# Optimization experiments

Hardware: AMD Instinct MI355X
Metric: run time of the kernel (lower is better)

The kernel has to match this reference:

```python
import jax, jax.numpy as jnp
import numpy as np

GAMMA_EPS = 0.05
ALPHA_POS = 4.0
ALPHA_NEG = 1.0

N, D, K_CLUSTERS = 262144, 128, 256


def setup_inputs() -> dict:
    key = jax.random.key(0)
    k1, k2, k3 = jax.random.split(key, 3)
    Xemb = jax.random.normal(k1, (N, D), dtype=jnp.float32)
    scores = jax.random.normal(k2, (N, K_CLUSTERS), dtype=jnp.float32)
    labels = jax.random.randint(k3, (N,), 0, K_CLUSTERS, dtype=jnp.int64)
    h_bias = jnp.asarray(0.1, dtype=jnp.float32)  # nn.Parameter(init_bias)
    return {"Xemb": Xemb, "scores": scores, "labels": labels,
            "h_bias": h_bias, "K": K_CLUSTERS}


def _bcl_forward(Xemb, scores, h_bias, labels, K):
    # labels are uniform in [0, K), so sorted unique labels == arange(K)
    # and the loop's k-index equals the label itself (pos_idx = labels).
    bias = jax.nn.softplus(h_bias)
    pos_bias = bias
    neg_bias = 9.0 * bias + GAMMA_EPS

    # scatter-mean centroids per cluster, then L2-normalize each centroid
    sums = jax.ops.segment_sum(Xemb, labels, num_segments=K)          # [K, D]
    counts = jax.ops.segment_sum(jnp.ones((Xemb.shape[0],), Xemb.dtype),
                                 labels, num_segments=K)              # [K]
    centroids = sums / counts[:, None]
    centroids = centroids / jnp.linalg.norm(centroids, axis=1, keepdims=True)

    x2 = jnp.sum(Xemb * Xemb, axis=1, keepdims=True)                  # [N, 1]
    c2 = jnp.sum(centroids * centroids, axis=1)                       # [K]
    XC_dist = x2 + c2[None, :] - 2.0 * (Xemb @ centroids.T)           # [N, K]

    # positive distance: gather own-cluster column
    pos_distances = jnp.take_along_axis(XC_dist, labels[:, None], axis=1)[:, 0]
    pos_sample_loss = jax.nn.relu(pos_distances - pos_bias)

    # min over negative clusters (exclude own column)
    own = jax.nn.one_hot(labels, K, dtype=jnp.bool_)
    min_neg = jnp.min(jnp.where(own, jnp.inf, XC_dist), axis=1)
    neg_sample_loss = jax.nn.relu(neg_bias - min_neg)

    pos_loss = jnp.mean(pos_sample_loss) * ALPHA_POS
    neg_loss = jnp.mean(neg_sample_loss) * ALPHA_NEG
    return jnp.stack([pos_loss, neg_loss])  # [ctrd_pos, ctrd_neg]


def reference(Xemb, scores, labels, h_bias, K):
    return _bcl_forward(Xemb, scores, h_bias, labels, K)
```

## Files before the change

kernel.cpp:

```cpp
#include <hip/hip_runtime.h>
#include <hip/hip_bf16.h>

#define DD 128
#define KK 256
#define TS 256
#define ROWB 136
#define SPB1 1024

typedef __attribute__((ext_vector_type(8))) short short8;
typedef __attribute__((ext_vector_type(4))) float f32x4;

static __device__ __forceinline__ unsigned short f2bf(float f) {
    unsigned int u = __float_as_uint(f);
    return (unsigned short)((u + 0x7fffu + ((u >> 16) & 1u)) >> 16);
}
static __device__ __forceinline__ float bf2f(unsigned short h) {
    return __uint_as_float(((unsigned int)h) << 16);
}

template<int MODE>
__global__ __launch_bounds__(1024) void k_stage1_gather(
    const float* __restrict__ X, const int* __restrict__ labels,
    float* __restrict__ partial)
{
    __shared__ int lab[SPB1];
    __shared__ int idx[SPB1];
    __shared__ int hist[KK];
    __shared__ int start[KK + 1];
    __shared__ int cursor[KK];

    const int tid  = threadIdx.x;
    const int lane = tid & 63;
    const int wave = tid >> 6;
    const int base = blockIdx.x * SPB1;

    if (tid < KK) hist[tid] = 0;
    __syncthreads();
    {
        const int l = labels[base + tid];
        lab[tid] = l;
        atomicAdd(&hist[l], 1);
    }
    __syncthreads();
    if (wave == 0) {
        const int h0 = hist[4*lane], h1 = hist[4*lane+1];
        const int h2 = hist[4*lane+2], h3 = hist[4*lane+3];
        const int s = h0 + h1 + h2 + h3;
        int t = s;
#pragma unroll
        for (int d = 1; d < 64; d <<= 1) { const int u = __shfl_up(t, d); if (lane >= d) t += u; }
        const int e = t - s;
        start[4*lane]   = e;
        start[4*lane+1] = e + h0;
        start[4*lane+2] = e + h0 + h1;
        start[4*lane+3] = e + h0 + h1 + h2;
        if (lane == 63) start[KK] = t;
    }
    __syncthreads();
    if (tid < KK) cursor[tid] = start[tid];
    __syncthreads();
    {
        const int pos = atomicAdd(&cursor[lab[tid]], 1);
        idx[pos] = tid;
    }
    __syncthreads();

    for (int c = wave; c < KK; c += 16) {
        const int s0 = start[c], s1 = start[c + 1];
        float2 acc = make_float2(0.f, 0.f);
        if (s1 > s0) {
            int n0 = idx[s0];
            float2 v = *(const float2*)(X + (size_t)(base + n0) * DD + 2 * lane);
            for (int i = s0 + 1; i < s1; ++i) {
                const int n1 = idx[i];
                const float2 v1 = *(const float2*)(X + (size_t)(base + n1) * DD + 2 * lane);
                acc.x += v.x; acc.y += v.y;
                n0 = n1; v = v1;
            }
            acc.x += v.x; acc.y += v.y;
        }
        if (MODE == 2) {
            atomicAdd(&partial[(size_t)c * DD + 2 * lane],     acc.x);
            atomicAdd(&partial[(size_t)c * DD + 2 * lane + 1], acc.y);
        } else {
            *(float2*)(partial + ((size_t)blockIdx.x * KK + c) * DD + 2 * lane) = acc;
        }
    }
}

__global__ void k_stage2(const float* __restrict__ partial, int nparts,
                         unsigned short* __restrict__ centb)
{
    const int k = blockIdx.x;
    const int t = threadIdx.x;
    const int d = t & (DD - 1);
    const int slice = t >> 7;
    float s = 0.f;
    for (int b = slice; b < nparts; b += 4)
        s += partial[((size_t)b * KK + k) * DD + d];
    __shared__ float red[4][DD];
    red[slice][d] = s;
    __syncthreads();
    float v = 0.f;
    if (t < DD) v = red[0][d] + red[1][d] + red[2][d] + red[3][d];
    float sq = v * v;
#pragma unroll
    for (int m = 32; m > 0; m >>= 1) sq += __shfl_xor(sq, m);
    __shared__ float wsum[8];
    if ((t & 63) == 0) wsum[t >> 6] = sq;
    __syncthreads();
    if (t < DD) centb[k * DD + d] = f2bf(v * rsqrtf(wsum[0] + wsum[1]));
}

__global__ __launch_bounds__(1024, 4) void k_stage3(
    const float* __restrict__ Xf, const int* __restrict__ labels,
    const unsigned short* __restrict__ centb,
    const float* __restrict__ hbias, float* __restrict__ loss, int spb)
{
    __shared__ unsigned short Cl[KK * ROWB];
    __shared__ unsigned short Xl[TS * ROWB];
    __shared__ int   labs[TS];
    __shared__ float lred[32];

    const int tid = threadIdx.x;
    const float hb = *hbias;
    const float bias = (hb > 20.f) ? hb : log1pf(__expf(hb));
    const float pos_bias = bias;
    const float neg_bias = 9.f * bias + 0.05f;

    const uint4* csrc = (const uint4*)centb;
    for (int c = tid; c < KK * DD / 8; c += 1024) {
        const int row = c >> 4;
        const int col = (c & 15) << 3;
        *(uint4*)(&Cl[row * ROWB + col]) = csrc[c];
    }

    const int lane = tid & 63;
    const int wave = tid >> 6;
    const int m15  = lane & 15;
    const int q    = lane >> 4;
    const int kq   = q << 3;
    const int base = blockIdx.x * spb;
    float pos_acc = 0.f, neg_acc = 0.f;

    for (int t0 = 0; t0 < spb; t0 += TS) {
        __syncthreads();
        const float4* xsrc = (const float4*)(Xf + (size_t)(base + t0) * DD);
        for (int c = tid; c < TS * DD / 4; c += 1024) {
            const int row = c >> 5;
            const int col = (c & 31) << 2;
            const float4 v = xsrc[c];
            ushort4 pk = make_ushort4(f2bf(v.x), f2bf(v.y), f2bf(v.z), f2bf(v.w));
            *(ushort4*)(&Xl[row * ROWB + col]) = pk;
        }
        if (tid < TS) labs[tid] = labels[base + t0 + tid];
        __syncthreads();

        short8 afrag[4];
        const int arow = (wave << 4) + m15;
#pragma unroll
        for (int s = 0; s < 4; ++s)
            afrag[s] = *(const short8*)(&Xl[arow * ROWB + (s << 5) + kq]);

        float x2p = 0.f;
#pragma unroll
        for (int s = 0; s < 4; ++s)
#pragma unroll
            for (int j = 0; j < 8; ++j) {
                const float e = bf2f((unsigned short)afrag[s][j]);
                x2p = fmaf(e, e, x2p);
            }
        x2p += __shfl_xor(x2p, 16);
        x2p += __shfl_xor(x2p, 32);

        f32x4 acc[16];
#pragma unroll
        for (int t = 0; t < 16; ++t) acc[t] = (f32x4){0.f, 0.f, 0.f, 0.f};
#pragma unroll
        for (int t = 0; t < 16; ++t) {
            const int brow = (t << 4) + m15;
#pragma unroll
            for (int s = 0; s < 4; ++s) {
                const short8 bfrag = *(const short8*)(&Cl[brow * ROWB + (s << 5) + kq]);
                acc[t] = __builtin_amdgcn_mfma_f32_16x16x32_bf16(afrag[s], bfrag, acc[t], 0, 0, 0);
            }
        }

#pragma unroll
        for (int r = 0; r < 4; ++r) {
            const int ml = (wave << 4) + (q << 2) + r;
            const int l  = labs[ml];
            const float x2 = __shfl(x2p, (q << 2) + r, 16);
            float posd = -1e30f, negd = -1e30f;
#pragma unroll
            for (int t = 0; t < 16; ++t) {
                const int cl = (t << 4) + m15;
                const float v = acc[t][r];
                const bool isp = (cl == l);
                posd = isp ? v : posd;
                negd = isp ? negd : fmaxf(negd, v);
            }
#pragma unroll
            for (int m = 1; m < 16; m <<= 1) {
                posd = fmaxf(posd, __shfl_xor(posd, m));
                negd = fmaxf(negd, __shfl_xor(negd, m));
            }
            if (m15 == 0) {
                const float pd = x2 + 1.0f - 2.f * posd;
                const float nd = x2 + 1.0f - 2.f * negd;
                pos_acc += fmaxf(pd - pos_bias, 0.f);
                neg_acc += fmaxf(neg_bias - nd, 0.f);
            }
        }
    }

#pragma unroll
    for (int m = 32; m > 0; m >>= 1) {
        pos_acc += __shfl_xor(pos_acc, m);
        neg_acc += __shfl_xor(neg_acc, m);
    }
    if (lane == 0) { lred[wave] = pos_acc; lred[16 + wave] = neg_acc; }
    __syncthreads();
    if (tid == 0) {
        float p = 0.f, n = 0.f;
#pragma unroll
        for (int w = 0; w < 16; ++w) { p += lred[w]; n += lred[16 + w]; }
        atomicAdd(&loss[0], p);
        atomicAdd(&loss[1], n);
    }
}

__global__ void k_final(const float* __restrict__ loss, float* __restrict__ out, float invN)
{
    if (threadIdx.x == 0) {
        out[0] = 4.0f * loss[0] * invN;
        out[1] = loss[1] * invN;
    }
}

extern "C" void kernel_launch(void* const* d_in, const int* in_sizes, int n_in,
                              void* d_out, int out_size, void* d_ws, size_t ws_size,
                              hipStream_t stream)
{
    const float* X      = (const float*)d_in[0];
    const int*   labels = (const int*)d_in[2];
    const float* hbias  = (const float*)d_in[3];
    float* out = (float*)d_out;
    const int N = in_sizes[0] / DD;
    const int G = N / SPB1;

    char* ws = (char*)d_ws;
    const size_t offC    = 256;
    const size_t offPart = offC + (size_t)KK * DD * 2;
    const size_t szPart  = (size_t)G * KK * DD * 4;

    float*          loss    = (float*)ws;
    unsigned short* centb   = (unsigned short*)(ws + offC);
    float*          partial = (float*)(ws + offPart);

    const int mode   = (ws_size >= offPart + szPart) ? 0 : 2;
    const int nparts = (mode == 2) ? 1 : G;

    hipMemsetAsync(loss, 0, 2 * sizeof(float), stream);
    if (mode == 2) hipMemsetAsync(partial, 0, (size_t)KK * DD * 4, stream);

    if (mode == 0) k_stage1_gather<0><<<G, 1024, 0, stream>>>(X, labels, partial);
    else           k_stage1_gather<2><<<G, 1024, 0, stream>>>(X, labels, partial);

    k_stage2<<<KK, 512, 0, stream>>>(partial, nparts, centb);

    k_stage3<<<G, 1024, 0, stream>>>(X, labels, centb, hbias, loss, N / G);

    k_final<<<1, 64, 0, stream>>>(loss, out, 1.0f / (float)N);
}
```

Measured before the change: 479.9 us.

## Emit bf16 X and row norms in stage1; stage3 uses 32x32 MFMA with prefetch

Stage 1 now writes a bf16 copy of X and per-row squared norms while it gathers rows for the centroid sums. Stage 3 reads that half-size bf16 copy and prefetches the next tile into registers, so it no longer converts fp32 X itself. It also moves from 16x16x32 to 32x32x16 MFMA with 512-thread blocks and uses DPP/swizzle max reductions. The extra writes in stage 1 and the larger workspace are paid to cut stage-3 traffic and conversion work; the x2 norm now comes from fp32 values rather than bf16-rounded ones.

```diff
diff --git a/kernel.cpp b/kernel.cpp
--- a/kernel.cpp
+++ b/kernel.cpp
@@ -8,20 +8,33 @@
 #define SPB1 1024
 
 typedef __attribute__((ext_vector_type(8))) short short8;
-typedef __attribute__((ext_vector_type(4))) float f32x4;
+typedef __attribute__((ext_vector_type(16))) float f32x16;
 
 static __device__ __forceinline__ unsigned short f2bf(float f) {
     unsigned int u = __float_as_uint(f);
     return (unsigned short)((u + 0x7fffu + ((u >> 16) & 1u)) >> 16);
 }
-static __device__ __forceinline__ float bf2f(unsigned short h) {
-    return __uint_as_float(((unsigned int)h) << 16);
+
+template<int CTRL>
+static __device__ __forceinline__ float mdpp_max(float x) {
+    const int xi = __builtin_bit_cast(int, x);
+    const int yi = __builtin_amdgcn_update_dpp(xi, xi, CTRL, 0xF, 0xF, false);
+    return fmaxf(x, __builtin_bit_cast(float, yi));
+}
+static __device__ __forceinline__ float redmax32(float x) {
+    x = mdpp_max<0xB1>(x);
+    x = mdpp_max<0x4E>(x);
+    x = mdpp_max<0x124>(x);
+    x = mdpp_max<0x128>(x);
+    const int yi = __builtin_amdgcn_ds_swizzle(__builtin_bit_cast(int, x), 0x401F);
+    return fmaxf(x, __builtin_bit_cast(float, yi));
 }
 
 template<int MODE>
 __global__ __launch_bounds__(1024) void k_stage1_gather(
     const float* __restrict__ X, const int* __restrict__ labels,
-    float* __restrict__ partial)
+    float* __restrict__ partial, unsigned int* __restrict__ Xbf,
+    float* __restrict__ x2g)
 {
     __shared__ int lab[SPB1];
     __shared__ int idx[SPB1];
@@ -75,9 +88,25 @@
                 const int n1 = idx[i];
                 const float2 v1 = *(const float2*)(X + (size_t)(base + n1) * DD + 2 * lane);
                 acc.x += v.x; acc.y += v.y;
+                if (MODE == 0) {
+                    Xbf[(size_t)(base + n0) * (DD/2) + lane] =
+                        ((unsigned)f2bf(v.y) << 16) | (unsigned)f2bf(v.x);
+                    float p = v.x*v.x + v.y*v.y;
+#pragma unroll
+                    for (int m = 32; m > 0; m >>= 1) p += __shfl_xor(p, m);
+                    if (lane == 0) x2g[base + n0] = p;
+                }
                 n0 = n1; v = v1;
             }
             acc.x += v.x; acc.y += v.y;
+            if (MODE == 0) {
+                Xbf[(size_t)(base + n0) * (DD/2) + lane] =
+                    ((unsigned)f2bf(v.y) << 16) | (unsigned)f2bf(v.x);
+                float p = v.x*v.x + v.y*v.y;
+#pragma unroll
+                for (int m = 32; m > 0; m >>= 1) p += __shfl_xor(p, m);
+                if (lane == 0) x2g[base + n0] = p;
+            }
         }
         if (MODE == 2) {
             atomicAdd(&partial[(size_t)c * DD + 2 * lane],     acc.x);
@@ -112,102 +141,148 @@
     if (t < DD) centb[k * DD + d] = f2bf(v * rsqrtf(wsum[0] + wsum[1]));
 }
 
-__global__ __launch_bounds__(1024, 4) void k_stage3(
-    const float* __restrict__ Xf, const int* __restrict__ labels,
+template<int XB>
+__global__ __launch_bounds__(512, 2) void k_stage3(
+    const float* __restrict__ Xf, const unsigned int* __restrict__ Xbf,
+    const int* __restrict__ labels, const float* __restrict__ x2g,
     const unsigned short* __restrict__ centb,
     const float* __restrict__ hbias, float* __restrict__ loss, int spb)
 {
-    __shared__ unsigned short Cl[KK * ROWB];
-    __shared__ unsigned short Xl[TS * ROWB];
-    __shared__ int   labs[TS];
-    __shared__ float lred[32];
-
-    const int tid = threadIdx.x;
+    __shared__ __align__(16) unsigned short Cl[KK * ROWB];
+    __shared__ __align__(16) unsigned short Xl[TS * ROWB];
+    __shared__ __align__(16) int   labsS[TS];
+    __shared__ __align__(16) float x2S[TS];
+    __shared__ float lred[16];
+
+    const int tid  = threadIdx.x;
+    const int lane = tid & 63;
+    const int wave = tid >> 6;
+    const int l31  = lane & 31;
+    const int half = lane >> 5;
+    const int base = blockIdx.x * spb;
+
     const float hb = *hbias;
     const float bias = (hb > 20.f) ? hb : log1pf(__expf(hb));
     const float pos_bias = bias;
     const float neg_bias = 9.f * bias + 0.05f;
 
-    const uint4* csrc = (const uint4*)centb;
-    for (int c = tid; c < KK * DD / 8; c += 1024) {
-        const int row = c >> 4;
-        const int col = (c & 15) << 3;
-        *(uint4*)(&Cl[row * ROWB + col]) = csrc[c];
-    }
-
-    const int lane = tid & 63;
-    const int wave = tid >> 6;
-    const int m15  = lane & 15;
-    const int q    = lane >> 4;
-    const int kq   = q << 3;
-    const int base = blockIdx.x * spb;
+    {
+        const uint4* csrc = (const uint4*)centb;
+        for (int c = tid; c < KK * DD / 8; c += 512) {
+            const int row = c >> 4, col = (c & 15) << 3;
+            *(uint4*)(&Cl[row * ROWB + col]) = csrc[c];
+        }
+    }
+
+    uint4 buf[8];
+    int labr = 0; float x2r = 0.f;
+    if (XB) {
+        const uint4* xs = (const uint4*)Xbf;
+        const size_t gb = (size_t)base << 4;
+#pragma unroll
+        for (int i = 0; i < 8; ++i) buf[i] = xs[gb + tid + (i << 9)];
+        if (tid < TS) { labr = labels[base + tid]; x2r = x2g[base + tid]; }
+    }
+
     float pos_acc = 0.f, neg_acc = 0.f;
 
     for (int t0 = 0; t0 < spb; t0 += TS) {
         __syncthreads();
-        const float4* xsrc = (const float4*)(Xf + (size_t)(base + t0) * DD);
-        for (int c = tid; c < TS * DD / 4; c += 1024) {
-            const int row = c >> 5;
-            const int col = (c & 31) << 2;
-            const float4 v = xsrc[c];
-            ushort4 pk = make_ushort4(f2bf(v.x), f2bf(v.y), f2bf(v.z), f2bf(v.w));
-            *(ushort4*)(&Xl[row * ROWB + col]) = pk;
-        }
-        if (tid < TS) labs[tid] = labels[base + t0 + tid];
-        __syncthreads();
-
-        short8 afrag[4];
-        const int arow = (wave << 4) + m15;
-#pragma unroll
-        for (int s = 0; s < 4; ++s)
-            afrag[s] = *(const short8*)(&Xl[arow * ROWB + (s << 5) + kq]);
-
-        float x2p = 0.f;
-#pragma unroll
-        for (int s = 0; s < 4; ++s)
-#pragma unroll
-            for (int j = 0; j < 8; ++j) {
-                const float e = bf2f((unsigned short)afrag[s][j]);
-                x2p = fmaf(e, e, x2p);
-            }
-        x2p += __shfl_xor(x2p, 16);
-        x2p += __shfl_xor(x2p, 32);
-
-        f32x4 acc[16];
-#pragma unroll
-        for (int t = 0; t < 16; ++t) acc[t] = (f32x4){0.f, 0.f, 0.f, 0.f};
-#pragma unroll
-        for (int t = 0; t < 16; ++t) {
-            const int brow = (t << 4) + m15;
-#pragma unroll
-            for (int s = 0; s < 4; ++s) {
-                const short8 bfrag = *(const short8*)(&Cl[brow * ROWB + (s << 5) + kq]);
-                acc[t] = __builtin_amdgcn_mfma_f32_16x16x32_bf16(afrag[s], bfrag, acc[t], 0, 0, 0);
-            }
-        }
-
-#pragma unroll
-        for (int r = 0; r < 4; ++r) {
-            const int ml = (wave << 4) + (q << 2) + r;
-            const int l  = labs[ml];
-            const float x2 = __shfl(x2p, (q << 2) + r, 16);
-            float posd = -1e30f, negd = -1e30f;
-#pragma unroll
-            for (int t = 0; t < 16; ++t) {
-                const int cl = (t << 4) + m15;
-                const float v = acc[t][r];
-                const bool isp = (cl == l);
-                posd = isp ? v : posd;
-                negd = isp ? negd : fmaxf(negd, v);
-            }
-#pragma unroll
-            for (int m = 1; m < 16; m <<= 1) {
-                posd = fmaxf(posd, __shfl_xor(posd, m));
-                negd = fmaxf(negd, __shfl_xor(negd, m));
-            }
-            if (m15 == 0) {
-                const float pd = x2 + 1.0f - 2.f * posd;
-                const float nd = x2 + 1.0f - 2.f * negd;
+
+        if (XB) {
+#pragma unroll
+            for (int i = 0; i < 8; ++i) {
+                const int c = tid + (i << 9);
+                const int row = c >> 4, col = (c & 15) << 3;
+                *(uint4*)(&Xl[row * ROWB + col]) = buf[i];
+            }
+            if (tid < TS) { labsS[tid] = labr; x2S[tid] = x2r; }
+            if (t0 + TS < spb) {
+                const uint4* xs = (const uint4*)Xbf;
+                const size_t gb = (size_t)(base + t0 + TS) << 4;
+#pragma unroll
+                for (int i = 0; i < 8; ++i) buf[i] = xs[gb + tid + (i << 9)];
+                if (tid < TS) {
+                    labr = labels[base + t0 + TS + tid];
+                    x2r  = x2g[base + t0 + TS + tid];
+                }
+            }
+            __syncthreads();
+        } else {
+            const float4* xsrc = (const float4*)(Xf + (size_t)(base + t0) * DD);
+            for (int c = tid; c < TS * DD / 4; c += 512) {
+                const int row = c >> 5, col = (c & 31) << 2;
+                const float4 v = xsrc[c];
+                ushort4 pk = make_ushort4(f2bf(v.x), f2bf(v.y), f2bf(v.z), f2bf(v.w));
+                *(ushort4*)(&Xl[row * ROWB + col]) = pk;
+            }
+            if (tid < TS) labsS[tid] = labels[base + t0 + tid];
+            __syncthreads();
+            {
+                const int s  = tid >> 1, h = tid & 1;
+                float p = 0.f;
+#pragma unroll
+                for (int c = 0; c < 8; ++c) {
+                    const short8 w = *(const short8*)(&Xl[s * ROWB + (h << 6) + (c << 3)]);
+#pragma unroll
+                    for (int j = 0; j < 8; ++j) {
+                        const float e = __uint_as_float(((unsigned)(unsigned short)w[j]) << 16);
+                        p = fmaf(e, e, p);
+                    }
+                }
+                p += __shfl_xor(p, 1);
+                if (h == 0 && s < TS) x2S[s] = p;
+            }
+            __syncthreads();
+        }
+
+        short8 af[8];
+        const int arow = (wave << 5) + l31;
+#pragma unroll
+        for (int s = 0; s < 8; ++s)
+            af[s] = *(const short8*)(&Xl[arow * ROWB + (s << 4) + (half << 3)]);
+
+        int la[16]; float xv[16];
+#pragma unroll
+        for (int g = 0; g < 4; ++g) {
+            const int r0 = (wave << 5) + (g << 3) + (half << 2);
+            const int4   L  = *(const int4*)(&labsS[r0]);
+            const float4 Xq = *(const float4*)(&x2S[r0]);
+            la[4*g+0] = L.x;  la[4*g+1] = L.y;  la[4*g+2] = L.z;  la[4*g+3] = L.w;
+            xv[4*g+0] = Xq.x; xv[4*g+1] = Xq.y; xv[4*g+2] = Xq.z; xv[4*g+3] = Xq.w;
+        }
+
+        float posc[16], negc[16];
+#pragma unroll
+        for (int r = 0; r < 16; ++r) { posc[r] = -1e30f; negc[r] = -1e30f; }
+
+#pragma unroll
+        for (int t = 0; t < 8; ++t) {
+            f32x16 acc;
+#pragma unroll
+            for (int r = 0; r < 16; ++r) acc[r] = 0.f;
+#pragma unroll
+            for (int s = 0; s < 8; ++s) {
+                const short8 bf = *(const short8*)(&Cl[(t*32 + l31) * ROWB + (s << 4) + (half << 3)]);
+                acc = __builtin_amdgcn_mfma_f32_32x32x16_bf16(af[s], bf, acc, 0, 0, 0);
+            }
+            const int myc = (t << 5) + l31;
+#pragma unroll
+            for (int r = 0; r < 16; ++r) {
+                const float v = acc[r];
+                const bool own = (la[r] == myc);
+                negc[r] = own ? negc[r] : fmaxf(negc[r], v);
+                posc[r] = own ? v : posc[r];
+            }
+        }
+
+#pragma unroll
+        for (int r = 0; r < 16; ++r) {
+            const float p  = redmax32(posc[r]);
+            const float nm = redmax32(negc[r]);
+            const float pd = xv[r] + 1.f - 2.f * p;
+            const float nd = xv[r] + 1.f - 2.f * nm;
+            if (l31 == r) {
                 pos_acc += fmaxf(pd - pos_bias, 0.f);
                 neg_acc += fmaxf(neg_bias - nd, 0.f);
             }
@@ -219,12 +294,12 @@
         pos_acc += __shfl_xor(pos_acc, m);
         neg_acc += __shfl_xor(neg_acc, m);
     }
-    if (lane == 0) { lred[wave] = pos_acc; lred[16 + wave] = neg_acc; }
+    if (lane == 0) { lred[wave] = pos_acc; lred[8 + wave] = neg_acc; }
     __syncthreads();
     if (tid == 0) {
         float p = 0.f, n = 0.f;
 #pragma unroll
-        for (int w = 0; w < 16; ++w) { p += lred[w]; n += lred[16 + w]; }
+        for (int w = 0; w < 8; ++w) { p += lred[w]; n += lred[8 + w]; }
         atomicAdd(&loss[0], p);
         atomicAdd(&loss[1], n);
     }
@@ -250,26 +325,32 @@
     const int G = N / SPB1;
 
     char* ws = (char*)d_ws;
-    const size_t offC    = 256;
-    const size_t offPart = offC + (size_t)KK * DD * 2;
-    const size_t szPart  = (size_t)G * KK * DD * 4;
+    const size_t offC   = 256;
+    const size_t offX2  = offC  + (size_t)KK * DD * 2;
+    const size_t offXbf = offX2 + (size_t)N * 4;
+    const size_t offP   = offXbf + (size_t)N * DD * 2;
+    const size_t szPart = (size_t)G * KK * DD * 4;
 
     float*          loss    = (float*)ws;
     unsigned short* centb   = (unsigned short*)(ws + offC);
-    float*          partial = (float*)(ws + offPart);
-
-    const int mode   = (ws_size >= offPart + szPart) ? 0 : 2;
-    const int nparts = (mode == 2) ? 1 : G;
+    float*          x2g     = (float*)(ws + offX2);
+    unsigned int*   Xbf     = (unsigned int*)(ws + offXbf);
+    float*          partial = (float*)(ws + offP);
+
+    const int full = (ws_size >= offP + szPart) ? 1 : 0;
+    const int nparts = full ? G : 1;
+    if (!full) partial = (float*)(ws + offC + (size_t)KK * DD * 2);
 
     hipMemsetAsync(loss, 0, 2 * sizeof(float), stream);
-    if (mode == 2) hipMemsetAsync(partial, 0, (size_t)KK * DD * 4, stream);
-
-    if (mode == 0) k_stage1_gather<0><<<G, 1024, 0, stream>>>(X, labels, partial);
-    else           k_stage1_gather<2><<<G, 1024, 0, stream>>>(X, labels, partial);
+    if (!full) hipMemsetAsync(partial, 0, (size_t)KK * DD * 4, stream);
+
+    if (full) k_stage1_gather<0><<<G, 1024, 0, stream>>>(X, labels, partial, Xbf, x2g);
+    else      k_stage1_gather<2><<<G, 1024, 0, stream>>>(X, labels, partial, nullptr, nullptr);
 
     k_stage2<<<KK, 512, 0, stream>>>(partial, nparts, centb);
 
-    k_stage3<<<G, 1024, 0, stream>>>(X, labels, centb, hbias, loss, N / G);
+    if (full) k_stage3<1><<<G, 512, 0, stream>>>(nullptr, Xbf, labels, x2g, centb, hbias, loss, N / G);
+    else      k_stage3<0><<<G, 512, 0, stream>>>(X, nullptr, labels, nullptr, centb, hbias, loss, N / G);
 
     k_final<<<1, 64, 0, stream>>>(loss, out, 1.0f / (float)N);
 }
```

Result: slower. 495.3 us (+3.2%).

## Prefetch gathered rows 8-deep across contiguous cluster ranges in segment-sum gather

Applied to the files above, without the earlier changes.

Each wave in the stage-1 gather now owns a contiguous block of 16 clusters rather than a strided set, and walks that block's sorted row indices as one stream. It keeps an 8-deep register ring of prefetched row loads and flushes the accumulator whenever a cluster boundary is crossed. The aim is more loads in flight per wave than the old 1-deep software pipeline, and no pipeline restart at each cluster. The cost is extra registers, a boundary check on every element, and wave loads that now depend on how many rows fall into each 16-cluster block.

```diff
diff --git a/kernel.cpp b/kernel.cpp
--- a/kernel.cpp
+++ b/kernel.cpp
@@ -65,26 +65,61 @@
     }
     __syncthreads();
 
-    for (int c = wave; c < KK; c += 16) {
-        const int s0 = start[c], s1 = start[c + 1];
-        float2 acc = make_float2(0.f, 0.f);
-        if (s1 > s0) {
-            int n0 = idx[s0];
-            float2 v = *(const float2*)(X + (size_t)(base + n0) * DD + 2 * lane);
-            for (int i = s0 + 1; i < s1; ++i) {
-                const int n1 = idx[i];
-                const float2 v1 = *(const float2*)(X + (size_t)(base + n1) * DD + 2 * lane);
-                acc.x += v.x; acc.y += v.y;
-                n0 = n1; v = v1;
+    const int c1 = (wave << 4) + 16;
+    int c = wave << 4;
+    const int s0 = start[c], s1 = start[c1];
+    const int cnt = s1 - s0;
+
+    float2 pf[8];
+#pragma unroll
+    for (int j = 0; j < 8; ++j)
+        if (j < cnt)
+            pf[j] = *(const float2*)(X + (size_t)(base + idx[s0 + j]) * DD + 2 * lane);
+
+    float2 acc = make_float2(0.f, 0.f);
+    int i = 0;
+    for (; i + 8 <= cnt; i += 8) {
+#pragma unroll
+        for (int j = 0; j < 8; ++j) {
+            const float2 v = pf[j];
+            if (i + j + 8 < cnt)
+                pf[j] = *(const float2*)(X + (size_t)(base + idx[s0 + i + j + 8]) * DD + 2 * lane);
+            while (s0 + i + j >= start[c + 1]) {
+                if (MODE == 2) {
+                    atomicAdd(&partial[(size_t)c * DD + 2*lane],     acc.x);
+                    atomicAdd(&partial[(size_t)c * DD + 2*lane + 1], acc.y);
+                } else {
+                    *(float2*)(partial + ((size_t)blockIdx.x * KK + c) * DD + 2*lane) = acc;
+                }
+                acc = make_float2(0.f, 0.f); ++c;
             }
             acc.x += v.x; acc.y += v.y;
         }
+    }
+#pragma unroll
+    for (int j = 0; j < 8; ++j) {
+        if (i + j < cnt) {
+            const float2 v = pf[j];
+            while (s0 + i + j >= start[c + 1]) {
+                if (MODE == 2) {
+                    atomicAdd(&partial[(size_t)c * DD + 2*lane],     acc.x);
+                    atomicAdd(&partial[(size_t)c * DD + 2*lane + 1], acc.y);
+                } else {
+                    *(float2*)(partial + ((size_t)blockIdx.x * KK + c) * DD + 2*lane) = acc;
+                }
+                acc = make_float2(0.f, 0.f); ++c;
+            }
+            acc.x += v.x; acc.y += v.y;
+        }
+    }
+    while (c < c1) {
         if (MODE == 2) {
-            atomicAdd(&partial[(size_t)c * DD + 2 * lane],     acc.x);
-            atomicAdd(&partial[(size_t)c * DD + 2 * lane + 1], acc.y);
+            atomicAdd(&partial[(size_t)c * DD + 2*lane],     acc.x);
+            atomicAdd(&partial[(size_t)c * DD + 2*lane + 1], acc.y);
         } else {
-            *(float2*)(partial + ((size_t)blockIdx.x * KK + c) * DD + 2 * lane) = acc;
-        }
+            *(float2*)(partial + ((size_t)blockIdx.x * KK + c) * DD + 2*lane) = acc;
+        }
+        acc = make_float2(0.f, 0.f); ++c;
     }
 }
 
```

Result: faster. 465.4 us (-3.0%).
